# Kernel tuning notes

Hardware: AMD Instinct MI355X
Metric: run time of the kernel (lower is better)

Reference implementation:

```python
import jax, jax.numpy as jnp
import numpy as np

N = 50000   # nodes
E = 800000  # edges (avg degree 16)
D = 64      # feature dim (in == out, so lin_self is Identity)
NEG_SLOPE = 0.2


def setup_inputs() -> dict:
    key = jax.random.key(0)
    ks = jax.random.split(key, 8)
    s = 1.0 / np.sqrt(D)
    return {
        "x": jax.random.normal(ks[0], (N, D), dtype=jnp.float32),
        "edge_index": jax.random.randint(ks[1], (2, E), 0, N, dtype=jnp.int64),
        "edge_attr": jax.random.uniform(ks[2], (E,), dtype=jnp.float32),
        "W_msg": jax.random.normal(ks[3], (D, D), dtype=jnp.float32) * s,
        "b_msg": jax.random.normal(ks[4], (D,), dtype=jnp.float32) * s,
        "W_edge": jax.random.normal(ks[5], (1, D), dtype=jnp.float32),
        "b_edge": jax.random.normal(ks[6], (D,), dtype=jnp.float32),
        "att": jax.random.normal(ks[7], (D,), dtype=jnp.float32) * s,
    }


def reference(x, edge_index, edge_attr, W_msg, b_msg, W_edge, b_edge, att):
    src, dst = edge_index[0], edge_index[1]
    # message: lin_msg(x_j) + lin_edge(edge_attr)           [E, D]
    msg = x[src] @ W_msg + b_msg + edge_attr[:, None] @ W_edge + b_edge
    # additive attention logits (heads=1)                   [E]
    logits = jnp.sum(jax.nn.leaky_relu(msg, NEG_SLOPE) * att, axis=-1)
    # segment softmax over destination nodes (PyG softmax, eps=1e-16)
    m = jax.ops.segment_max(logits, dst, num_segments=N)
    m = jnp.where(jnp.isneginf(m), 0.0, m)
    ex = jnp.exp(logits - m[dst])
    denom = jax.ops.segment_sum(ex, dst, num_segments=N)
    alpha = ex / (denom[dst] + 1e-16)
    weighted = msg * alpha[:, None]
    # scatter-max aggregation; empty segments -> 0 (PyG fill value)
    agg = jax.ops.segment_max(weighted, dst, num_segments=N)
    agg = jnp.where(jnp.isneginf(agg), 0.0, agg)
    # lin_self is Identity (in_channels == out_channels, skip_linear=False)
    return agg + x
```

## Files before the change

kernel.cpp:

```cpp
#include <hip/hip_runtime.h>

#define N_NODES 50000
#define N_EDGES 800000
#define DIM 64
#define NEG_SLOPE 0.2f
#define NEG_INF (-__builtin_inff())
#define NB      3125
#define NBIN    782
#define SEGS    8
#define SEGCAP  384
#define LMAX    64
#define HB      196
#define EPB     4096

typedef _Float16 half8 __attribute__((ext_vector_type(8)));

__global__ __launch_bounds__(256) void k_pre(const float* __restrict__ x,
                                             const float* __restrict__ W,
                                             const float* __restrict__ b_msg,
                                             const float* __restrict__ b_edge,
                                             _Float16* __restrict__ xmh,
                                             const int* __restrict__ eidx,
                                             const float* __restrict__ eattr,
                                             unsigned* __restrict__ tails,
                                             int2* __restrict__ rec) {
    __shared__ float Ws[DIM * DIM];
    __shared__ float xs[16 * DIM];
    __shared__ unsigned hb[NBIN];
    int tid = threadIdx.x;
    int bid = blockIdx.x;
    bool heavy = bid < HB;

    unsigned xcc;
    asm volatile("s_getreg_b32 %0, hwreg(HW_REG_XCC_ID, 0, 4)" : "=s"(xcc));
    int seg = (int)(xcc & 7u);

    if (heavy)
        for (int b = tid; b < NBIN; b += 256) hb[b] = 0;

    const float4* W4 = (const float4*)W;
    float4* Ws4 = (float4*)Ws;
    #pragma unroll
    for (int i = 0; i < 4; ++i) Ws4[tid + 256 * i] = W4[tid + 256 * i];
    int base = bid * 16;
    ((float4*)xs)[tid] = ((const float4*)(x + (size_t)base * DIM))[tid];
    __syncthreads();

    unsigned rl[16];
    if (heavy) {
        int ebase = bid * EPB;
        #pragma unroll
        for (int j = 0; j < 16; ++j) {
            int e = ebase + j * 256 + tid;
            rl[j] = 0xFFFFFFFFu;
            if (e < N_EDGES) {
                int edst = eidx[N_EDGES + e];
                unsigned bin = (unsigned)edst >> 6;
                unsigned r = atomicAdd(&hb[bin], 1u);
                rl[j] = r | (bin << 12) | ((unsigned)(edst & 63) << 22);
            }
        }
    }
    __syncthreads();

    if (heavy) {
        for (int b = tid; b < NBIN; b += 256) {
            unsigned h = hb[b];
            if (h) hb[b] = atomicAdd(tails + (seg * NBIN + b), h);
        }
    }

    int w = tid >> 6;
    int d = tid & 63;
    float bias = b_msg[d] + b_edge[d];
    float s0 = bias, s1 = bias, s2 = bias, s3 = bias;
    const float* xr = xs + (w * 4) * DIM;
    #pragma unroll
    for (int k = 0; k < DIM; ++k) {
        float wv = Ws[k * DIM + d];
        s0 = fmaf(xr[k], wv, s0);
        s1 = fmaf(xr[DIM + k], wv, s1);
        s2 = fmaf(xr[2 * DIM + k], wv, s2);
        s3 = fmaf(xr[3 * DIM + k], wv, s3);
    }
    _Float16* o = xmh + ((size_t)base + w * 4) * DIM + d;
    o[0] = (_Float16)s0;
    o[DIM] = (_Float16)s1;
    o[2 * DIM] = (_Float16)s2;
    o[3 * DIM] = (_Float16)s3;

    __syncthreads();

    if (heavy) {
        int ebase = bid * EPB;
        #pragma unroll
        for (int j = 0; j < 16; ++j) {
            unsigned u = rl[j];
            if (u != 0xFFFFFFFFu) {
                int e = ebase + j * 256 + tid;
                int esrc  = eidx[e];
                float ea  = eattr[e];
                unsigned bin  = (u >> 12) & 0x3FFu;
                unsigned slot = hb[bin] + (u & 0xFFFu);
                if (slot < SEGCAP)
                    rec[(size_t)(seg * NBIN + bin) * SEGCAP + slot] =
                        make_int2((esrc << 6) | (int)(u >> 22),
                                  __float_as_int(ea));
            }
        }
    }
}

__global__ __launch_bounds__(256) void k_aggregate(const half8* __restrict__ xm8,
                                                   const int2* __restrict__ rec,
                                                   const unsigned* __restrict__ tails,
                                                   const float4* __restrict__ W_edge4,
                                                   const float4* __restrict__ att4,
                                                   const float4* __restrict__ x4,
                                                   float4* __restrict__ out4) {
    __shared__ int2 lst[32 * LMAX];
    __shared__ unsigned degs[32];
    __shared__ unsigned scnt[SEGS];
    int tid  = threadIdx.x;
    int bin  = blockIdx.x >> 1;
    int half = blockIdx.x & 1;

    if (tid < SEGS) {
        unsigned c = tails[tid * NBIN + bin];
        scnt[tid] = c > SEGCAP ? SEGCAP : c;
    }
    if (tid < 32) degs[tid] = 0;
    __syncthreads();

    for (int s = 0; s < SEGS * SEGCAP; s += 256) {
        int slot = s + tid;
        int sg = slot / SEGCAP, i = slot % SEGCAP;
        if ((unsigned)i < scnt[sg]) {
            int2 r = rec[(size_t)(sg * NBIN + bin) * SEGCAP + i];
            unsigned nr = (unsigned)r.x & 63u;
            if ((int)(nr >> 5) == half) {
                unsigned k = atomicAdd(&degs[nr & 31u], 1u);
                if (k < LMAX) lst[(nr & 31u) * LMAX + k] = r;
            }
        }
    }
    __syncthreads();

    int lane = tid & 63;
    int wvi  = tid >> 6;
    int g = lane >> 3, t = lane & 7;
    int rr = wvi * 8 + g;
    int node = bin * 64 + half * 32 + rr;
    if (node >= N_NODES) return;

    unsigned deg = degs[rr];
    if (deg > LMAX) deg = LMAX;
    size_t obase = (size_t)node * 16 + 2 * t;
    if (deg == 0) {
        out4[obase] = x4[obase];
        out4[obase + 1] = x4[obase + 1];
        return;
    }
    float4 wa = W_edge4[2 * t], wb = W_edge4[2 * t + 1];
    float4 aa = att4[2 * t],    ab = att4[2 * t + 1];
    float we[8] = {wa.x, wa.y, wa.z, wa.w, wb.x, wb.y, wb.z, wb.w};
    float at[8] = {aa.x, aa.y, aa.z, aa.w, ab.x, ab.y, ab.z, ab.w};

    const int2* L = lst + rr * LMAX;
    int2 r = L[0];
    float ea = __int_as_float(r.y);
    half8 h  = xm8[(size_t)((unsigned)r.x >> 6) * 8 + t];

    float m = NEG_INF, denom = 0.f;
    float v[8];
    #pragma unroll
    for (int k = 0; k < 8; ++k) v[k] = 0.f;

    unsigned i = 0;
    while (true) {
        bool more = (i + 1) < deg;
        float ea2; half8 h2;
        if (more) {
            int2 r2 = L[i + 1];
            ea2 = __int_as_float(r2.y);
            h2  = xm8[(size_t)((unsigned)r2.x >> 6) * 8 + t];
        }
        float msg[8];
        float p = 0.f;
        #pragma unroll
        for (int k = 0; k < 8; ++k) {
            float f = (float)h[k];
            msg[k] = fmaf(ea, we[k], f);
            float lr = fmaxf(msg[k], NEG_SLOPE * msg[k]);
            p = fmaf(lr, at[k], p);
        }
        p += __shfl_xor(p, 1, 64);
        p += __shfl_xor(p, 2, 64);
        p += __shfl_xor(p, 4, 64);
        if (i == 0) {
            m = p; denom = 1.f;
            #pragma unroll
            for (int k = 0; k < 8; ++k) v[k] = msg[k];
        } else {
            float M  = fmaxf(m, p);
            float so = __expf(m - M);
            float sn = __expf(p - M);
            denom = fmaf(denom, so, sn);
            #pragma unroll
            for (int k = 0; k < 8; ++k)
                v[k] = fmaxf(v[k] * so, msg[k] * sn);
            m = M;
        }
        if (!more) break;
        ea = ea2; h = h2; ++i;
    }
    float inv = 1.0f / (denom + 1e-16f);
    float4 xa = x4[obase], xb = x4[obase + 1];
    float4 r0, r1;
    r0.x = fmaf(v[0], inv, xa.x);
    r0.y = fmaf(v[1], inv, xa.y);
    r0.z = fmaf(v[2], inv, xa.z);
    r0.w = fmaf(v[3], inv, xa.w);
    r1.x = fmaf(v[4], inv, xb.x);
    r1.y = fmaf(v[5], inv, xb.y);
    r1.z = fmaf(v[6], inv, xb.z);
    r1.w = fmaf(v[7], inv, xb.w);
    out4[obase] = r0;
    out4[obase + 1] = r1;
}

extern "C" void kernel_launch(void* const* d_in, const int* in_sizes, int n_in,
                              void* d_out, int out_size, void* d_ws, size_t ws_size,
                              hipStream_t stream) {
    const float* x      = (const float*)d_in[0];
    const int*   eidx   = (const int*)d_in[1];
    const float* eattr  = (const float*)d_in[2];
    const float* W_msg  = (const float*)d_in[3];
    const float* b_msg  = (const float*)d_in[4];
    const float* W_edge = (const float*)d_in[5];
    const float* b_edge = (const float*)d_in[6];
    const float* att    = (const float*)d_in[7];
    float* out = (float*)d_out;

    _Float16* xmh   = (_Float16*)d_ws;
    int2*     rec   = (int2*)(xmh + (size_t)N_NODES * DIM);
    unsigned* tails = (unsigned*)(rec + (size_t)SEGS * NBIN * SEGCAP);

    hipMemsetAsync(tails, 0, (size_t)SEGS * NBIN * 4, stream);

    k_pre<<<NB, 256, 0, stream>>>(x, W_msg, b_msg, b_edge, xmh,
                                  eidx, eattr, tails, rec);
    k_aggregate<<<NBIN * 2, 256, 0, stream>>>(
        (const half8*)xmh, rec, tails, (const float4*)W_edge,
        (const float4*)att, (const float4*)x, (float4*)out);
}
```

Before: 125.3 us.

## Process whole 64-node bin per 512-thread block instead of two half-blocks

The aggregate kernel now uses one 512-thread block per 64-node bin rather than two 256-thread blocks that each scanned all records of the bin and kept only half. Each edge record is now read once instead of twice. The record scan also walks each segment only up to its actual count, which removes the division and modulo and the loop over empty capacity slots. The trade-off is larger blocks with twice the shared memory and half as many blocks, which may reduce occupancy and load balance.

```diff
diff --git a/kernel.cpp b/kernel.cpp
--- a/kernel.cpp
+++ b/kernel.cpp
@@ -111,37 +111,34 @@
     }
 }
 
-__global__ __launch_bounds__(256) void k_aggregate(const half8* __restrict__ xm8,
+__global__ __launch_bounds__(512) void k_aggregate(const half8* __restrict__ xm8,
                                                    const int2* __restrict__ rec,
                                                    const unsigned* __restrict__ tails,
                                                    const float4* __restrict__ W_edge4,
                                                    const float4* __restrict__ att4,
                                                    const float4* __restrict__ x4,
                                                    float4* __restrict__ out4) {
-    __shared__ int2 lst[32 * LMAX];
-    __shared__ unsigned degs[32];
+    __shared__ int2 lst[64 * LMAX];
+    __shared__ unsigned degs[64];
     __shared__ unsigned scnt[SEGS];
-    int tid  = threadIdx.x;
-    int bin  = blockIdx.x >> 1;
-    int half = blockIdx.x & 1;
+    int tid = threadIdx.x;
+    int bin = blockIdx.x;
 
     if (tid < SEGS) {
         unsigned c = tails[tid * NBIN + bin];
         scnt[tid] = c > SEGCAP ? SEGCAP : c;
     }
-    if (tid < 32) degs[tid] = 0;
-    __syncthreads();
-
-    for (int s = 0; s < SEGS * SEGCAP; s += 256) {
-        int slot = s + tid;
-        int sg = slot / SEGCAP, i = slot % SEGCAP;
-        if ((unsigned)i < scnt[sg]) {
-            int2 r = rec[(size_t)(sg * NBIN + bin) * SEGCAP + i];
+    if (tid < 64) degs[tid] = 0;
+    __syncthreads();
+
+    for (int sg = 0; sg < SEGS; ++sg) {
+        unsigned c = scnt[sg];
+        const int2* R = rec + (size_t)(sg * NBIN + bin) * SEGCAP;
+        for (unsigned i = tid; i < c; i += 512) {
+            int2 r = R[i];
             unsigned nr = (unsigned)r.x & 63u;
-            if ((int)(nr >> 5) == half) {
-                unsigned k = atomicAdd(&degs[nr & 31u], 1u);
-                if (k < LMAX) lst[(nr & 31u) * LMAX + k] = r;
-            }
+            unsigned k = atomicAdd(&degs[nr], 1u);
+            if (k < LMAX) lst[nr * LMAX + k] = r;
         }
     }
     __syncthreads();
@@ -150,7 +147,7 @@
     int wvi  = tid >> 6;
     int g = lane >> 3, t = lane & 7;
     int rr = wvi * 8 + g;
-    int node = bin * 64 + half * 32 + rr;
+    int node = bin * 64 + rr;
     if (node >= N_NODES) return;
 
     unsigned deg = degs[rr];
@@ -216,17 +213,17 @@
     }
     float inv = 1.0f / (denom + 1e-16f);
     float4 xa = x4[obase], xb = x4[obase + 1];
-    float4 r0, r1;
-    r0.x = fmaf(v[0], inv, xa.x);
-    r0.y = fmaf(v[1], inv, xa.y);
-    r0.z = fmaf(v[2], inv, xa.z);
-    r0.w = fmaf(v[3], inv, xa.w);
-    r1.x = fmaf(v[4], inv, xb.x);
-    r1.y = fmaf(v[5], inv, xb.y);
-    r1.z = fmaf(v[6], inv, xb.z);
-    r1.w = fmaf(v[7], inv, xb.w);
-    out4[obase] = r0;
-    out4[obase + 1] = r1;
+    float4 q0, q1;
+    q0.x = fmaf(v[0], inv, xa.x);
+    q0.y = fmaf(v[1], inv, xa.y);
+    q0.z = fmaf(v[2], inv, xa.z);
+    q0.w = fmaf(v[3], inv, xa.w);
+    q1.x = fmaf(v[4], inv, xb.x);
+    q1.y = fmaf(v[5], inv, xb.y);
+    q1.z = fmaf(v[6], inv, xb.z);
+    q1.w = fmaf(v[7], inv, xb.w);
+    out4[obase] = q0;
+    out4[obase + 1] = q1;
 }
 
 extern "C" void kernel_launch(void* const* d_in, const int* in_sizes, int n_in,
@@ -250,7 +247,7 @@
 
     k_pre<<<NB, 256, 0, stream>>>(x, W_msg, b_msg, b_edge, xmh,
                                   eidx, eattr, tails, rec);
-    k_aggregate<<<NBIN * 2, 256, 0, stream>>>(
+    k_aggregate<<<NBIN, 512, 0, stream>>>(
         (const half8*)xmh, rec, tails, (const float4*)W_edge,
         (const float4*)att, (const float4*)x, (float4*)out);
 }
```

Result: slower. 128.4 us (+2.4%).
